# Kernel optimization log

Measured on AMD Instinct MI355X. Metric: run time of the kernel, lower is better.

The kernel has to match this reference:

```python
import jax, jax.numpy as jnp
import numpy as np

B, S, D, H = 2, 2048, 1024, 16
HD = D // H
SCALE = HD ** -0.5

def setup_inputs() -> dict:
    key = jax.random.key(0)
    ks = jax.random.split(key, 5)
    x = jax.random.normal(ks[0], (B, S, D), dtype=jnp.float32)
    Wqkv = jax.random.normal(ks[1], (D, 3 * D), dtype=jnp.float32) * (D ** -0.5)
    bqkv = jnp.zeros((3 * D,), dtype=jnp.float32)
    Wproj = jax.random.normal(ks[2], (D, D), dtype=jnp.float32) * (D ** -0.5)
    bproj = jnp.zeros((D,), dtype=jnp.float32)
    return {"x": x, "Wqkv": Wqkv, "bqkv": bqkv, "Wproj": Wproj, "bproj": bproj}

def reference(x, Wqkv, bqkv, Wproj, bproj):
    b, s, _ = x.shape
    qkv = x @ Wqkv + bqkv                       # [B,S,3D]
    qkv = qkv.reshape(b, s, 3, H, HD)
    q, k, v = [jnp.transpose(qkv[:, :, i], (0, 2, 1, 3)) for i in range(3)]  # [B,H,S,HD]
    attn = jnp.einsum('bhqd,bhkd->bhqk', q, k) * SCALE   # [B,H,S,S]
    attn = jax.nn.softmax(attn, axis=-1)
    out = jnp.einsum('bhqk,bhkd->bhqd', attn, v)         # [B,H,S,HD]
    out = jnp.transpose(out, (0, 2, 1, 3)).reshape(b, s, D)
    return out @ Wproj + bproj
```

## Files before the change

### kernel.cpp

```cpp
#include <hip/hip_runtime.h>
#include <hip/hip_bf16.h>

#define BB 2
#define SS 2048
#define DD 1024
#define HH 16
#define HDD 64
#define MM (BB*SS)
#define NQKV (3*DD)
#define SCALE 0.125f
#define QPRESCALE 0.18033688f

typedef __bf16 bf16_t;
typedef bf16_t bf16x4 __attribute__((ext_vector_type(4)));
typedef bf16_t bf16x8 __attribute__((ext_vector_type(8)));
typedef float f32x4 __attribute__((ext_vector_type(4)));
typedef float f32x16 __attribute__((ext_vector_type(16)));

__device__ __forceinline__ void gl_lds16(const bf16_t* g, bf16_t* l) {
    __builtin_amdgcn_global_load_lds(
        (const __attribute__((address_space(1))) unsigned int*)(uintptr_t)g,
        (__attribute__((address_space(3))) unsigned int*)(uintptr_t)l,
        16, 0, 0);
}

__device__ __forceinline__ f32x4 MF(bf16x8 a, bf16x8 b, f32x4 c) {
    return __builtin_amdgcn_mfma_f32_16x16x32_bf16(a, b, c, 0, 0, 0);
}

__global__ __launch_bounds__(256) void prep(
    const float* __restrict__ x, const float* __restrict__ Wqkv,
    const float* __restrict__ Wproj, bf16_t* __restrict__ xb,
    bf16_t* __restrict__ wqkvt, bf16_t* __restrict__ wprojt)
{
    const int bx = blockIdx.x;
    if (bx < 2048) {
        int i = (bx * 256 + threadIdx.x) * 8;
        float4 a = *(const float4*)(x + i);
        float4 b = *(const float4*)(x + i + 4);
        bf16x8 v;
        v[0]=(bf16_t)a.x; v[1]=(bf16_t)a.y; v[2]=(bf16_t)a.z; v[3]=(bf16_t)a.w;
        v[4]=(bf16_t)b.x; v[5]=(bf16_t)b.y; v[6]=(bf16_t)b.z; v[7]=(bf16_t)b.w;
        *reinterpret_cast<bf16x8*>(xb + i) = v;
        return;
    }
    __shared__ float tile[32][33];
    const float* src; bf16_t* dst; int C, bxl, byl;
    if (bx < 5120) {
        int t = bx - 2048;
        byl = t / 96; bxl = t - byl * 96;
        src = Wqkv;  dst = wqkvt;  C = NQKV;
    } else {
        int t = bx - 5120;
        byl = t >> 5; bxl = t & 31;
        src = Wproj; dst = wprojt; C = DD;
    }
    const int R = DD;
    const int tx = threadIdx.x & 31, ty = threadIdx.x >> 5;
    const int r0 = byl * 32, c0 = bxl * 32;
    #pragma unroll
    for (int i = 0; i < 32; i += 8)
        tile[ty + i][tx] = src[(size_t)(r0 + ty + i) * C + c0 + tx];
    __syncthreads();
    #pragma unroll
    for (int i = 0; i < 32; i += 8)
        dst[(size_t)(c0 + ty + i) * R + r0 + tx] = (bf16_t)tile[tx][ty + i];
}

__global__ __launch_bounds__(512, 2) void gemm_qkv(
    const bf16_t* __restrict__ A, const bf16_t* __restrict__ Bt,
    const float* __restrict__ bias,
    bf16_t* __restrict__ qw, bf16_t* __restrict__ kw, bf16_t* __restrict__ vtw)
{
    constexpr int K  = DD;
    constexpr int BM = 256, BN = 192, BK = 32;
    constexpr int NT = K / BK;

    __shared__ __align__(16) bf16_t smem[50176];
    bf16_t* const Ab[3] = { smem, smem + 8192, smem + 16384 };
    bf16_t* const Bb[3] = { smem + 24576, smem + 30720, smem + 36864 };

    const int tid  = threadIdx.x;
    const int w    = tid >> 6;
    const int lane = tid & 63;
    const int lr   = lane & 15;
    const int quad = lane >> 4;
    const int wm   = w >> 2;
    const int wn   = w & 3;

    const int flat = blockIdx.y * 16 + blockIdx.x;
    const int swz  = (flat & 7) * 32 + (flat >> 3);
    const int m0   = (swz >> 4) * BM;
    const int n0   = (swz & 15) * BN;

    f32x4 acc[8][3];
    #pragma unroll
    for (int mi = 0; mi < 8; mi++)
        #pragma unroll
        for (int ni = 0; ni < 3; ni++)
            acc[mi][ni] = (f32x4){0.f, 0.f, 0.f, 0.f};

    const int ca0 = tid,        ca1 = tid + 512;
    const int cb0 = tid,        cb1 = tid + 256;
    const bf16_t* aG0 = A  + (size_t)(m0 + (ca0 >> 2)) * K + (ca0 & 3) * 8;
    const bf16_t* aG1 = A  + (size_t)(m0 + (ca1 >> 2)) * K + (ca1 & 3) * 8;
    const bf16_t* bG0 = Bt + (size_t)(n0 + (cb0 >> 2)) * K + (cb0 & 3) * 8;
    const bf16_t* bG1 = Bt + (size_t)(n0 + (cb1 >> 2)) * K + (cb1 & 3) * 8;

    auto stage = [&](int kt, bf16_t* Ad, bf16_t* Bd) {
        const int ko = kt * BK;
        gl_lds16(aG0 + ko, Ad + ca0 * 8);
        gl_lds16(aG1 + ko, Ad + ca1 * 8);
        gl_lds16(bG0 + ko, Bd + cb0 * 8);
        gl_lds16(bG1 + ko, Bd + cb1 * 8);
    };

    stage(0, Ab[0], Bb[0]);
    stage(1, Ab[1], Bb[1]);
    asm volatile("s_waitcnt vmcnt(4)" ::: "memory");
    __builtin_amdgcn_s_barrier();
    __builtin_amdgcn_sched_barrier(0);

    const int aOff = (wm * 128 + lr) * BK + quad * 8;
    const int bOff = (wn * 48  + lr) * BK + quad * 8;

    auto tileStep = [&](int t, const bf16_t* Ac, const bf16_t* Bc,
                        bf16_t* An, bf16_t* Bn) {
        bf16x8 af[8], bk[3];
        #pragma unroll
        for (int mi = 0; mi < 8; mi++)
            af[mi] = *(const bf16x8*)(Ac + aOff + mi * 16 * BK);
        #pragma unroll
        for (int ni = 0; ni < 3; ni++)
            bk[ni] = *(const bf16x8*)(Bc + bOff + ni * 16 * BK);
        if (t < NT - 2) stage(t + 2, An, Bn);
        __builtin_amdgcn_sched_barrier(0);
        __builtin_amdgcn_s_setprio(1);
        #pragma unroll
        for (int mi = 0; mi < 8; mi++)
            #pragma unroll
            for (int ni = 0; ni < 3; ni++)
                acc[mi][ni] = MF(af[mi], bk[ni], acc[mi][ni]);
        __builtin_amdgcn_s_setprio(0);
        __builtin_amdgcn_sched_barrier(0);
        if (t < NT - 2)       asm volatile("s_waitcnt vmcnt(4)" ::: "memory");
        else if (t == NT - 2) asm volatile("s_waitcnt vmcnt(0)" ::: "memory");
        __builtin_amdgcn_s_barrier();
        __builtin_amdgcn_sched_barrier(0);
    };

    #pragma unroll 1
    for (int tt = 0; tt < NT - 2; tt += 3) {
        tileStep(tt,     Ab[0], Bb[0], Ab[2], Bb[2]);
        tileStep(tt + 1, Ab[1], Bb[1], Ab[0], Bb[0]);
        tileStep(tt + 2, Ab[2], Bb[2], Ab[1], Bb[1]);
    }
    tileStep(NT - 2, Ab[0], Bb[0], nullptr, nullptr);
    tileStep(NT - 1, Ab[1], Bb[1], nullptr, nullptr);

    __builtin_amdgcn_s_barrier();

    const int colBase = n0 + wn * 48;
    const int vbase   = (n0 < 2048) ? 2048 : n0;
    #pragma unroll
    for (int mi = 0; mi < 8; mi++) {
        const int rl0 = wm * 128 + mi * 16 + quad * 4;
        #pragma unroll
        for (int ni = 0; ni < 3; ni++) {
            const int col = colBase + ni * 16 + lr;
            const float bcol = bias[col];
            const int which = col >> 10;
            const int d = col & 1023;
            const int h = d >> 6, hd = d & 63;
            if (which == 0) {
                #pragma unroll
                for (int reg = 0; reg < 4; reg++) {
                    const int row = m0 + rl0 + reg;
                    const int b = row >> 11, s = row & 2047;
                    qw[(((size_t)(b * HH + h)) * SS + s) * HDD + hd] =
                        (bf16_t)((acc[mi][ni][reg] + bcol) * QPRESCALE);
                }
            } else if (which == 1) {
                #pragma unroll
                for (int reg = 0; reg < 4; reg++) {
                    const int row = m0 + rl0 + reg;
                    const int b = row >> 11, s = row & 2047;
                    kw[(((size_t)(b * HH + h)) * SS + s) * HDD + hd] =
                        (bf16_t)(acc[mi][ni][reg] + bcol);
                }
            } else {
                bf16x4 pk;
                #pragma unroll
                for (int reg = 0; reg < 4; reg++)
                    pk[reg] = (bf16_t)(acc[mi][ni][reg] + bcol);
                const int lc = col - vbase;
                *reinterpret_cast<bf16x4*>(&smem[lc * 260 + rl0]) = pk;
            }
        }
    }
    const int nv = n0 + BN - 2048;
    if (nv > 0) {
        __builtin_amdgcn_s_barrier();
        const int nvc = nv < BN ? nv : BN;
        const int lcb = tid >> 5;
        const int rl  = (tid & 31) * 8;
        const int b   = m0 >> 11;
        const int s   = (m0 & 2047) + rl;
        for (int j = 0; j < nvc / 16; j++) {
            const int lc = j * 16 + lcb;
            bf16x8 vv = *reinterpret_cast<const bf16x8*>(&smem[lc * 260 + rl]);
            const int col = vbase + lc;
            const int d = col & 1023;
            const int h = d >> 6, hd = d & 63;
            *reinterpret_cast<bf16x8*>(
                vtw + (((size_t)(b * HH + h)) * HDD + hd) * SS + s) = vv;
        }
    }
}

__global__ __launch_bounds__(256) void gemm_bt64(
    const bf16_t* __restrict__ A, const bf16_t* __restrict__ Bt,
    const float* __restrict__ bias, float* __restrict__ outf, int N, int K)
{
    __shared__ __align__(16) bf16_t As[2][64 * 32];
    __shared__ __align__(16) bf16_t Bs[2][128 * 32];

    const int tid  = threadIdx.x;
    const int w    = tid >> 6;
    const int lane = tid & 63;
    const int lr   = lane & 15;
    const int quad = lane >> 4;
    const int m0   = blockIdx.y * 64;
    const int n0   = blockIdx.x * 128;
    const int wm   = w >> 1;
    const int wn   = w & 1;

    f32x4 acc[2][4];
    #pragma unroll
    for (int i = 0; i < 2; i++)
        #pragma unroll
        for (int j = 0; j < 4; j++) acc[i][j] = (f32x4){0.f, 0.f, 0.f, 0.f};

    const int stgRow = lane >> 2;
    const int stgCol = (lane & 3) * 8;
    const bf16_t* aPtr = A  + (size_t)(m0 + w * 16 + stgRow) * K + stgCol;
    const bf16_t* bPtr = Bt + (size_t)(n0 + w * 32 + stgRow) * K + stgCol;
    const size_t rowSkip = (size_t)16 * K;

    for (int ks = 0; ks < K; ks += 64) {
        __syncthreads();
        #pragma unroll
        for (int s = 0; s < 2; s++) {
            const int ko = ks + s * 32;
            gl_lds16(aPtr + ko,           &As[s][w * 512]);
            gl_lds16(bPtr + ko,           &Bs[s][w * 1024]);
            gl_lds16(bPtr + rowSkip + ko, &Bs[s][w * 1024 + 512]);
        }
        __syncthreads();

        #pragma unroll
        for (int s = 0; s < 2; s++) {
            bf16x8 af[2], bf[4];
            #pragma unroll
            for (int mi = 0; mi < 2; mi++)
                af[mi] = *reinterpret_cast<const bf16x8*>(&As[s][(wm * 32 + mi * 16 + lr) * 32 + quad * 8]);
            #pragma unroll
            for (int ni = 0; ni < 4; ni++)
                bf[ni] = *reinterpret_cast<const bf16x8*>(&Bs[s][(wn * 64 + ni * 16 + lr) * 32 + quad * 8]);
            #pragma unroll
            for (int mi = 0; mi < 2; mi++)
                #pragma unroll
                for (int ni = 0; ni < 4; ni++)
                    acc[mi][ni] = __builtin_amdgcn_mfma_f32_16x16x32_bf16(af[mi], bf[ni], acc[mi][ni], 0, 0, 0);
        }
    }

    #pragma unroll
    for (int mi = 0; mi < 2; mi++)
        #pragma unroll
        for (int ni = 0; ni < 4; ni++)
            #pragma unroll
            for (int reg = 0; reg < 4; reg++) {
                int row = m0 + wm * 32 + mi * 16 + quad * 4 + reg;
                int col = n0 + wn * 64 + ni * 16 + lr;
                outf[(size_t)row * N + col] = acc[mi][ni][reg] + bias[col];
            }
}

__global__ __launch_bounds__(512, 4) void attn_kernel(
    const bf16_t* __restrict__ qws, const bf16_t* __restrict__ kws,
    const bf16_t* __restrict__ vtws, bf16_t* __restrict__ ob)
{
    __shared__ __align__(16) bf16_t smem[35072];
    bf16_t* Ks = smem;
    bf16_t* Vs = smem + 16640;

    const int tid  = threadIdx.x;
    const int w    = tid >> 6;
    const int g    = w >> 2;
    const int wg   = w & 3;
    const int lane = tid & 63;
    const int ln31 = lane & 31;
    const int ln5  = lane >> 5;

    const int flat = blockIdx.y * 16 + blockIdx.x;
    const int t2 = flat >> 3;
    const int bh = (t2 >> 4) * 8 + (flat & 7);
    const int qb = t2 & 15;
    const int b  = bh >> 4;
    const int h  = bh & 15;

    const bf16_t* Qh  = qws  + (size_t)bh * SS * HDD;
    const bf16_t* Kh  = kws  + (size_t)bh * SS * HDD;
    const bf16_t* Vth = vtws + (size_t)bh * HDD * SS;

    const int q0w    = qb * 128 + wg * 32;
    const int kvbase = g * 1024;

    bf16x8 aq[4];
    #pragma unroll
    for (int f = 0; f < 4; f++)
        aq[f] = *(const bf16x8*)(Qh + (size_t)(q0w + ln31) * HDD + f * 16 + ln5 * 8);

    const int gtid = tid & 255;
    const int sc = gtid & 7;
    const int sr = gtid >> 3;
    const int vcol = (sc >> 1) * 16 + (sc & 1) * 4;

    {
        const int ko = g * 520;
        const int vo = g * 4608;
        bf16x8 k0 = *(const bf16x8*)(Kh  + (size_t)(kvbase + sr     ) * HDD + sc * 8);
        bf16x8 k1 = *(const bf16x8*)(Kh  + (size_t)(kvbase + sr + 32) * HDD + sc * 8);
        bf16x8 v0 = *(const bf16x8*)(Vth + (size_t)(sr     ) * SS + kvbase + sc * 8);
        bf16x8 v1 = *(const bf16x8*)(Vth + (size_t)(sr + 32) * SS + kvbase + sc * 8);
        *reinterpret_cast<bf16x8*>(&Ks[(ko + sc * 65 + sr     ) * 8]) = k0;
        *reinterpret_cast<bf16x8*>(&Ks[(ko + sc * 65 + sr + 32) * 8]) = k1;
        bf16_t* vd0 = &Vs[vo + (sr     ) * 72 + vcol];
        bf16_t* vd1 = &Vs[vo + (sr + 32) * 72 + vcol];
        *reinterpret_cast<bf16x4*>(vd0)     = __builtin_shufflevector(v0, v0, 0,1,2,3);
        *reinterpret_cast<bf16x4*>(vd0 + 8) = __builtin_shufflevector(v0, v0, 4,5,6,7);
        *reinterpret_cast<bf16x4*>(vd1)     = __builtin_shufflevector(v1, v1, 0,1,2,3);
        *reinterpret_cast<bf16x4*>(vd1 + 8) = __builtin_shufflevector(v1, v1, 4,5,6,7);
    }
    __syncthreads();

    float l = 0.f;
    f32x16 o[2];
    #pragma unroll
    for (int nh = 0; nh < 2; nh++)
        #pragma unroll
        for (int r = 0; r < 16; r++) o[nh][r] = 0.f;

    int buf = 0;
    for (int it = 0; it < 16; ++it) {
        const int ko = buf * 1040 + g * 520;
        const int vo = buf * 9216 + g * 4608;

        f32x16 sfr[2];
        __builtin_amdgcn_s_setprio(1);
        #pragma unroll
        for (int ni = 0; ni < 2; ni++) {
            #pragma unroll
            for (int r = 0; r < 16; r++) sfr[ni][r] = 0.f;
            #pragma unroll
            for (int f = 0; f < 4; f++) {
                bf16x8 kb = *reinterpret_cast<const bf16x8*>(
                    &Ks[(ko + (2 * f + ln5) * 65 + ni * 32 + ln31) * 8]);
                sfr[ni] = __builtin_amdgcn_mfma_f32_32x32x16_bf16(kb, aq[f], sfr[ni], 0, 0, 0);
            }
        }
        __builtin_amdgcn_s_setprio(0);

        bf16x8 nk0, nk1, nv0, nv1;
        const bool more = (it + 1 < 16);
        if (more) {
            const int kvn = kvbase + (it + 1) * 64;
            nk0 = *(const bf16x8*)(Kh  + (size_t)(kvn + sr     ) * HDD + sc * 8);
            nk1 = *(const bf16x8*)(Kh  + (size_t)(kvn + sr + 32) * HDD + sc * 8);
            nv0 = *(const bf16x8*)(Vth + (size_t)(sr     ) * SS + kvn + sc * 8);
            nv1 = *(const bf16x8*)(Vth + (size_t)(sr + 32) * SS + kvn + sc * 8);
        }

        float p[2][16];
        #pragma unroll
        for (int ni = 0; ni < 2; ni++)
            #pragma unroll
            for (int r = 0; r < 16; r++) {
                p[ni][r] = __builtin_amdgcn_exp2f(sfr[ni][r]);
                l += p[ni][r];
            }

        bf16x8 ap[4];
        #pragma unroll
        for (int c16 = 0; c16 < 4; c16++)
            #pragma unroll
            for (int j = 0; j < 8; j++)
                ap[c16][j] = (bf16_t)p[c16 >> 1][(c16 & 1) * 8 + j];

        __builtin_amdgcn_s_setprio(1);
        #pragma unroll
        for (int nh = 0; nh < 2; nh++) {
            const bf16_t* vrow = &Vs[vo + (nh * 32 + ln31) * 72];
            #pragma unroll
            for (int c16 = 0; c16 < 4; c16++) {
                bf16x8 vb = *reinterpret_cast<const bf16x8*>(vrow + c16 * 16 + 8 * ln5);
                o[nh] = __builtin_amdgcn_mfma_f32_32x32x16_bf16(ap[c16], vb, o[nh], 0, 0, 0);
            }
        }
        __builtin_amdgcn_s_setprio(0);

        if (more) {
            const int ko1 = (buf ^ 1) * 1040 + g * 520;
            const int vo1 = (buf ^ 1) * 9216 + g * 4608;
            *reinterpret_cast<bf16x8*>(&Ks[(ko1 + sc * 65 + sr     ) * 8]) = nk0;
            *reinterpret_cast<bf16x8*>(&Ks[(ko1 + sc * 65 + sr + 32) * 8]) = nk1;
            bf16_t* vd0 = &Vs[vo1 + (sr     ) * 72 + vcol];
            bf16_t* vd1 = &Vs[vo1 + (sr + 32) * 72 + vcol];
            *reinterpret_cast<bf16x4*>(vd0)     = __builtin_shufflevector(nv0, nv0, 0,1,2,3);
            *reinterpret_cast<bf16x4*>(vd0 + 8) = __builtin_shufflevector(nv0, nv0, 4,5,6,7);
            *reinterpret_cast<bf16x4*>(vd1)     = __builtin_shufflevector(nv1, nv1, 0,1,2,3);
            *reinterpret_cast<bf16x4*>(vd1 + 8) = __builtin_shufflevector(nv1, nv1, 4,5,6,7);
        }
        __syncthreads();
        buf ^= 1;
    }

    l += __shfl_xor(l, 32, 64);

    __syncthreads();
    float* Of = (float*)smem;
    float* Lf = (float*)(smem + 16384);
    if (ln5 == 0) Lf[g * 128 + wg * 32 + ln31] = l;
    if (g == 1) {
        #pragma unroll
        for (int nh = 0; nh < 2; nh++)
            #pragma unroll
            for (int r = 0; r < 16; r++) {
                const int q = (r & 3) + 8 * (r >> 2) + 4 * ln5;
                Of[(wg * 32 + q) * 64 + nh * 32 + ln31] = o[nh][r];
            }
    }
    __syncthreads();
    if (g == 0) {
        float inv[16];
        #pragma unroll
        for (int r = 0; r < 16; r++) {
            const int q = (r & 3) + 8 * (r >> 2) + 4 * ln5;
            inv[r] = 1.f / (Lf[wg * 32 + q] + Lf[128 + wg * 32 + q]);
        }
        #pragma unroll
        for (int nh = 0; nh < 2; nh++)
            #pragma unroll
            for (int r = 0; r < 16; r++) {
                const int q  = (r & 3) + 8 * (r >> 2) + 4 * ln5;
                const int hd = nh * 32 + ln31;
                float val = (o[nh][r] + Of[(wg * 32 + q) * 64 + hd]) * inv[r];
                ob[((size_t)b * SS + q0w + q) * DD + h * HDD + hd] = (bf16_t)val;
            }
    }
}

extern "C" void kernel_launch(void* const* d_in, const int* in_sizes, int n_in,
                              void* d_out, int out_size, void* d_ws, size_t ws_size,
                              hipStream_t stream) {
    const float* x     = (const float*)d_in[0];
    const float* Wqkv  = (const float*)d_in[1];
    const float* bqkv  = (const float*)d_in[2];
    const float* Wproj = (const float*)d_in[3];
    const float* bproj = (const float*)d_in[4];
    float* out = (float*)d_out;

    const size_t NEL = (size_t)MM * DD;
    bf16_t* qws    = (bf16_t*)d_ws;
    bf16_t* kws    = qws  + NEL;
    bf16_t* vtws   = kws  + NEL;
    bf16_t* xb     = vtws + NEL;
    bf16_t* ows    = xb;
    bf16_t* wqkvt  = xb + NEL;
    bf16_t* wprojt = wqkvt + (size_t)NQKV * DD;

    prep<<<6144, 256, 0, stream>>>(x, Wqkv, Wproj, xb, wqkvt, wprojt);

    gemm_qkv<<<dim3(NQKV / 192, MM / 256), 512, 0, stream>>>(
        xb, wqkvt, bqkv, qws, kws, vtws);

    attn_kernel<<<dim3(SS / 128, BB * HH), 512, 0, stream>>>(qws, kws, vtws, ows);

    gemm_bt64<<<dim3(DD / 128, MM / 64), 256, 0, stream>>>(
        ows, wprojt, bproj, out, DD, DD);
}
```

Baseline: 172.4 us.

## Rewrite projection GEMM with triple-buffered async pipeline and hoist attention prefetch

Replaces the output projection GEMM with a 128x128-tile, 512-thread kernel that triple-buffers K tiles loaded directly into LDS, issuing the next load before each tile's MFMAs and waiting with explicit vmcnt counts. It also swizzles block order for L2 reuse and hoists the bias load. In the attention kernel, the global prefetch of the next K/V tile is moved ahead of the QK^T MFMAs so memory latency overlaps compute. The change relies on an MF helper defined elsewhere and on hand-placed waitcnt and barriers, which could stall if the counts are wrong.

After: 172.3 us. No clear change (-0.0%).

```diff
diff --git a/kernel.cpp b/kernel.cpp
--- a/kernel.cpp
+++ b/kernel.cpp
@@ -218,73 +218,103 @@
     }
 }
 
-__global__ __launch_bounds__(256) void gemm_bt64(
+__global__ __launch_bounds__(512, 6) void gemm_proj(
     const bf16_t* __restrict__ A, const bf16_t* __restrict__ Bt,
-    const float* __restrict__ bias, float* __restrict__ outf, int N, int K)
+    const float* __restrict__ bias, float* __restrict__ outf)
 {
-    __shared__ __align__(16) bf16_t As[2][64 * 32];
-    __shared__ __align__(16) bf16_t Bs[2][128 * 32];
+    constexpr int K  = DD;
+    constexpr int N  = DD;
+    constexpr int BM = 128, BN = 128, BK = 32;
+    constexpr int NT = K / BK;
+
+    __shared__ __align__(16) bf16_t smem[24576];
+    bf16_t* const Ab[3] = { smem, smem + 4096, smem + 8192 };
+    bf16_t* const Bb[3] = { smem + 12288, smem + 16384, smem + 20480 };
 
     const int tid  = threadIdx.x;
     const int w    = tid >> 6;
     const int lane = tid & 63;
     const int lr   = lane & 15;
     const int quad = lane >> 4;
-    const int m0   = blockIdx.y * 64;
-    const int n0   = blockIdx.x * 128;
-    const int wm   = w >> 1;
-    const int wn   = w & 1;
-
-    f32x4 acc[2][4];
-    #pragma unroll
-    for (int i = 0; i < 2; i++)
-        #pragma unroll
-        for (int j = 0; j < 4; j++) acc[i][j] = (f32x4){0.f, 0.f, 0.f, 0.f};
-
-    const int stgRow = lane >> 2;
-    const int stgCol = (lane & 3) * 8;
-    const bf16_t* aPtr = A  + (size_t)(m0 + w * 16 + stgRow) * K + stgCol;
-    const bf16_t* bPtr = Bt + (size_t)(n0 + w * 32 + stgRow) * K + stgCol;
-    const size_t rowSkip = (size_t)16 * K;
-
-    for (int ks = 0; ks < K; ks += 64) {
-        __syncthreads();
-        #pragma unroll
-        for (int s = 0; s < 2; s++) {
-            const int ko = ks + s * 32;
-            gl_lds16(aPtr + ko,           &As[s][w * 512]);
-            gl_lds16(bPtr + ko,           &Bs[s][w * 1024]);
-            gl_lds16(bPtr + rowSkip + ko, &Bs[s][w * 1024 + 512]);
-        }
-        __syncthreads();
-
-        #pragma unroll
-        for (int s = 0; s < 2; s++) {
-            bf16x8 af[2], bf[4];
-            #pragma unroll
-            for (int mi = 0; mi < 2; mi++)
-                af[mi] = *reinterpret_cast<const bf16x8*>(&As[s][(wm * 32 + mi * 16 + lr) * 32 + quad * 8]);
-            #pragma unroll
-            for (int ni = 0; ni < 4; ni++)
-                bf[ni] = *reinterpret_cast<const bf16x8*>(&Bs[s][(wn * 64 + ni * 16 + lr) * 32 + quad * 8]);
-            #pragma unroll
-            for (int mi = 0; mi < 2; mi++)
-                #pragma unroll
-                for (int ni = 0; ni < 4; ni++)
-                    acc[mi][ni] = __builtin_amdgcn_mfma_f32_16x16x32_bf16(af[mi], bf[ni], acc[mi][ni], 0, 0, 0);
-        }
-    }
-
-    #pragma unroll
-    for (int mi = 0; mi < 2; mi++)
-        #pragma unroll
-        for (int ni = 0; ni < 4; ni++)
+    const int wm   = w >> 2;
+    const int wn   = w & 3;
+
+    const int flat = blockIdx.y * 8 + blockIdx.x;
+    const int swz  = (flat & 7) * 32 + (flat >> 3);
+    const int m0   = (swz >> 3) * BM;
+    const int n0   = (swz & 7) * BN;
+
+    f32x4 acc[4][2];
+    #pragma unroll
+    for (int mi = 0; mi < 4; mi++)
+        #pragma unroll
+        for (int ni = 0; ni < 2; ni++)
+            acc[mi][ni] = (f32x4){0.f, 0.f, 0.f, 0.f};
+
+    const bf16_t* aG = A  + (size_t)(m0 + (tid >> 2)) * K + (tid & 3) * 8;
+    const bf16_t* bG = Bt + (size_t)(n0 + (tid >> 2)) * K + (tid & 3) * 8;
+
+    auto stage = [&](int kt, bf16_t* Ad, bf16_t* Bd) {
+        const int ko = kt * BK;
+        gl_lds16(aG + ko, Ad + tid * 8);
+        gl_lds16(bG + ko, Bd + tid * 8);
+    };
+
+    stage(0, Ab[0], Bb[0]);
+    stage(1, Ab[1], Bb[1]);
+    asm volatile("s_waitcnt vmcnt(2)" ::: "memory");
+    __builtin_amdgcn_s_barrier();
+    __builtin_amdgcn_sched_barrier(0);
+
+    const int aOff = (wm * 64 + lr) * BK + quad * 8;
+    const int bOff = (wn * 32 + lr) * BK + quad * 8;
+
+    auto tileStep = [&](int t, const bf16_t* Ac, const bf16_t* Bc,
+                        bf16_t* An, bf16_t* Bn) {
+        bf16x8 af[4], bk[2];
+        #pragma unroll
+        for (int mi = 0; mi < 4; mi++)
+            af[mi] = *(const bf16x8*)(Ac + aOff + mi * 16 * BK);
+        #pragma unroll
+        for (int ni = 0; ni < 2; ni++)
+            bk[ni] = *(const bf16x8*)(Bc + bOff + ni * 16 * BK);
+        if (t < NT - 2) stage(t + 2, An, Bn);
+        __builtin_amdgcn_sched_barrier(0);
+        __builtin_amdgcn_s_setprio(1);
+        #pragma unroll
+        for (int mi = 0; mi < 4; mi++)
+            #pragma unroll
+            for (int ni = 0; ni < 2; ni++)
+                acc[mi][ni] = MF(af[mi], bk[ni], acc[mi][ni]);
+        __builtin_amdgcn_s_setprio(0);
+        __builtin_amdgcn_sched_barrier(0);
+        if (t < NT - 2)       asm volatile("s_waitcnt vmcnt(2)" ::: "memory");
+        else if (t == NT - 2) asm volatile("s_waitcnt vmcnt(0)" ::: "memory");
+        __builtin_amdgcn_s_barrier();
+        __builtin_amdgcn_sched_barrier(0);
+    };
+
+    #pragma unroll 1
+    for (int tt = 0; tt < NT - 2; tt += 3) {
+        tileStep(tt,     Ab[0], Bb[0], Ab[2], Bb[2]);
+        tileStep(tt + 1, Ab[1], Bb[1], Ab[0], Bb[0]);
+        tileStep(tt + 2, Ab[2], Bb[2], Ab[1], Bb[1]);
+    }
+    tileStep(NT - 2, Ab[0], Bb[0], nullptr, nullptr);
+    tileStep(NT - 1, Ab[1], Bb[1], nullptr, nullptr);
+
+    #pragma unroll
+    for (int mi = 0; mi < 4; mi++)
+        #pragma unroll
+        for (int ni = 0; ni < 2; ni++) {
+            const int col = n0 + wn * 32 + ni * 16 + lr;
+            const float bcol = bias[col];
             #pragma unroll
             for (int reg = 0; reg < 4; reg++) {
-                int row = m0 + wm * 32 + mi * 16 + quad * 4 + reg;
-                int col = n0 + wn * 64 + ni * 16 + lr;
-                outf[(size_t)row * N + col] = acc[mi][ni][reg] + bias[col];
-            }
+                const int row = m0 + wm * 64 + mi * 16 + quad * 4 + reg;
+                outf[(size_t)row * N + col] = acc[mi][ni][reg] + bcol;
+            }
+        }
 }
 
 __global__ __launch_bounds__(512, 4) void attn_kernel(
@@ -357,21 +387,6 @@
         const int ko = buf * 1040 + g * 520;
         const int vo = buf * 9216 + g * 4608;
 
-        f32x16 sfr[2];
-        __builtin_amdgcn_s_setprio(1);
-        #pragma unroll
-        for (int ni = 0; ni < 2; ni++) {
-            #pragma unroll
-            for (int r = 0; r < 16; r++) sfr[ni][r] = 0.f;
-            #pragma unroll
-            for (int f = 0; f < 4; f++) {
-                bf16x8 kb = *reinterpret_cast<const bf16x8*>(
-                    &Ks[(ko + (2 * f + ln5) * 65 + ni * 32 + ln31) * 8]);
-                sfr[ni] = __builtin_amdgcn_mfma_f32_32x32x16_bf16(kb, aq[f], sfr[ni], 0, 0, 0);
-            }
-        }
-        __builtin_amdgcn_s_setprio(0);
-
         bf16x8 nk0, nk1, nv0, nv1;
         const bool more = (it + 1 < 16);
         if (more) {
@@ -381,6 +396,21 @@
             nv0 = *(const bf16x8*)(Vth + (size_t)(sr     ) * SS + kvn + sc * 8);
             nv1 = *(const bf16x8*)(Vth + (size_t)(sr + 32) * SS + kvn + sc * 8);
         }
+
+        f32x16 sfr[2];
+        __builtin_amdgcn_s_setprio(1);
+        #pragma unroll
+        for (int ni = 0; ni < 2; ni++) {
+            #pragma unroll
+            for (int r = 0; r < 16; r++) sfr[ni][r] = 0.f;
+            #pragma unroll
+            for (int f = 0; f < 4; f++) {
+                bf16x8 kb = *reinterpret_cast<const bf16x8*>(
+                    &Ks[(ko + (2 * f + ln5) * 65 + ni * 32 + ln31) * 8]);
+                sfr[ni] = __builtin_amdgcn_mfma_f32_32x32x16_bf16(kb, aq[f], sfr[ni], 0, 0, 0);
+            }
+        }
+        __builtin_amdgcn_s_setprio(0);
 
         float p[2][16];
         #pragma unroll
@@ -487,6 +517,6 @@
 
     attn_kernel<<<dim3(SS / 128, BB * HH), 512, 0, stream>>>(qws, kws, vtws, ows);
 
-    gemm_bt64<<<dim3(DD / 128, MM / 64), 256, 0, stream>>>(
-        ows, wprojt, bproj, out, DD, DD);
-}
+    gemm_proj<<<dim3(DD / 128, MM / 128), 512, 0, stream>>>(
+        ows, wprojt, bproj, out);
+}
```
